# Kernel optimization log

Hardware: AMD Instinct MI355X
Metric: run time of the kernel (lower is better)

## Reference

```python
import jax, jax.numpy as jnp
import numpy as np

BETA = 0.1
GAMMA = 0.5
LABEL_SMOOTHING = 0.0
IGNORE_INDEX = -100

B, T, H, V = 8, 512, 2048, 32000  # B = 2 * num_pairs (first half chosen, second half rejected)


def setup_inputs() -> dict:
    key = jax.random.key(0)
    k1, k2, k3, k4 = jax.random.split(key, 4)
    lin_weight = jax.random.normal(k1, (V, H), dtype=jnp.float32) * 0.02
    _input = jax.random.normal(k2, (B, T, H), dtype=jnp.float32)
    target = jax.random.randint(k3, (B, T), 0, V, dtype=jnp.int64)
    # sprinkle some ignore_index positions like padded labels
    pad = jax.random.uniform(k4, (B, T)) < 0.1
    target = jnp.where(pad, IGNORE_INDEX, target)
    bias = jax.random.normal(k4, (V,), dtype=jnp.float32) * 0.02
    return {"lin_weight": lin_weight, "_input": _input, "target": target, "bias": bias}


def reference(lin_weight, _input, target, bias):
    # fused linear -> log_softmax over vocab
    logits = jnp.einsum("bth,vh->btv", _input, lin_weight) + bias  # (B, T, V)
    logps = jax.nn.log_softmax(logits.astype(jnp.float32), axis=-1)
    # gather target log-probs, masking ignore_index
    mask = (target != IGNORE_INDEX)
    tgt = jnp.where(mask, target, 0)
    per_token_logps = jnp.take_along_axis(logps, tgt[..., None], axis=-1)[..., 0]
    per_token_logps = per_token_logps * mask  # (B, T)
    # SimPO uses length-normalized (average) sequence log-prob
    avg_logps = per_token_logps.sum(-1) / jnp.maximum(mask.sum(-1), 1)  # (B,)
    n_pairs = B // 2
    chosen_logps = avg_logps[:n_pairs]
    rejected_logps = avg_logps[n_pairs:]
    d = BETA * (chosen_logps - rejected_logps) - GAMMA
    loss = (-jax.nn.log_sigmoid(d) * (1.0 - LABEL_SMOOTHING)
            - jax.nn.log_sigmoid(-d) * LABEL_SMOOTHING).sum() / n_pairs
    return loss
```

## Files before the change

### kernel.cpp

```cpp
#include <hip/hip_runtime.h>
#include <stdint.h>
#include <math.h>

constexpr int Bb = 8, Tt = 512, Hh = 2048, Vv = 32000;
constexpr int M = Bb * Tt;
constexpr int K = Hh;
constexpr int N = Vv;
constexpr int NB = N / 128;
constexpr int BK = 32;
constexpr int KITERS = K / BK;
constexpr int IGNORE = -100;

typedef __attribute__((ext_vector_type(8))) short bf16x8;
typedef __attribute__((ext_vector_type(4))) float f32x4;

__device__ inline void gld16(const void* g, const void* l) {
  __builtin_amdgcn_global_load_lds(
      (const __attribute__((address_space(1))) uint32_t*)g,
      (__attribute__((address_space(3))) uint32_t*)l, 16, 0, 0);
}

__device__ inline unsigned short f2bf(float f) {
  union { float f; unsigned u; } x; x.f = f;
  unsigned r = x.u + 0x7fffu + ((x.u >> 16) & 1u);
  return (unsigned short)(r >> 16);
}

__global__ void cast_bf16_kernel(const float* __restrict__ src,
                                 unsigned short* __restrict__ dst, int n4) {
  int i = blockIdx.x * blockDim.x + threadIdx.x;
  int stride = gridDim.x * blockDim.x;
  const float4* s4 = (const float4*)src;
  ushort4* d4 = (ushort4*)dst;
  for (; i < n4; i += stride) {
    float4 v = s4[i];
    ushort4 o;
    o.x = f2bf(v.x); o.y = f2bf(v.y); o.z = f2bf(v.z); o.w = f2bf(v.w);
    d4[i] = o;
  }
}

__global__ __launch_bounds__(256, 4)
void gemm_stats(const unsigned short* __restrict__ X,
                const unsigned short* __restrict__ W,
                const float* __restrict__ bias,
                const int* __restrict__ tgt,
                float* __restrict__ m_part,
                float* __restrict__ s_part,
                float* __restrict__ tlogit) {
  __shared__ __align__(16) unsigned short As0[128 * BK];
  __shared__ __align__(16) unsigned short As1[128 * BK];
  __shared__ __align__(16) unsigned short Bs0[128 * BK];
  __shared__ __align__(16) unsigned short Bs1[128 * BK];
  __shared__ float red_m[2][128];
  __shared__ float red_s[2][128];

  const int tid = threadIdx.x;
  const int lane = tid & 63;
  const int wid = tid >> 6;
  const int waveM = wid >> 1;
  const int waveN = wid & 1;
  const int q = lane >> 4;
  const int c = lane & 15;
  const int bm = blockIdx.x;
  const int bn = blockIdx.y;

  const int strow = tid >> 2;
  const int schunk = (lane & 3) ^ ((lane >> 2) & 3);
  const unsigned short* gA = X + (size_t)(bm * 128 + strow) * K + schunk * 8;
  const unsigned short* gB = W + (size_t)(bn * 128 + strow) * K + schunk * 8;
  const int dRow = wid * 16;

  int offA[4], offB[4];
#pragma unroll
  for (int i = 0; i < 4; ++i) {
    const int rA = waveM * 64 + i * 16 + c;
    const int rB = waveN * 64 + i * 16 + c;
    offA[i] = rA * BK + ((q ^ (rA & 3)) * 8);
    offB[i] = rB * BK + ((q ^ (rB & 3)) * 8);
  }

  f32x4 acc[4][4];
#pragma unroll
  for (int i = 0; i < 4; ++i)
#pragma unroll
    for (int j = 0; j < 4; ++j) acc[i][j] = (f32x4){0.f, 0.f, 0.f, 0.f};

  auto stage = [&](unsigned short* Ad, unsigned short* Bd, int tile) {
    const size_t k0 = (size_t)tile * BK;
#pragma unroll
    for (int j = 0; j < 2; ++j) {
      gld16(gA + (size_t)j * 64 * K + k0, Ad + (j * 64 + dRow) * BK);
      gld16(gB + (size_t)j * 64 * K + k0, Bd + (j * 64 + dRow) * BK);
    }
  };
  auto compute = [&](const unsigned short* Asb, const unsigned short* Bsb) {
    bf16x8 af[4], bfr[4];
#pragma unroll
    for (int i = 0; i < 4; ++i) {
      af[i]  = *(const bf16x8*)(Asb + offA[i]);
      bfr[i] = *(const bf16x8*)(Bsb + offB[i]);
    }
#pragma unroll
    for (int mi = 0; mi < 4; ++mi)
#pragma unroll
      for (int ni = 0; ni < 4; ++ni)
        acc[mi][ni] = __builtin_amdgcn_mfma_f32_16x16x32_bf16(
            af[mi], bfr[ni], acc[mi][ni], 0, 0, 0);
  };

  stage(As0, Bs0, 0);

  for (int i2 = 0; i2 < KITERS / 2 - 1; ++i2) {
    __syncthreads();
    stage(As1, Bs1, 2 * i2 + 1);
    compute(As0, Bs0);
    __syncthreads();
    stage(As0, Bs0, 2 * i2 + 2);
    compute(As1, Bs1);
  }
  __syncthreads();
  stage(As1, Bs1, KITERS - 1);
  compute(As0, Bs0);
  __syncthreads();
  compute(As1, Bs1);

  const int colBase = bn * 128 + waveN * 64;
  float bvals[4];
#pragma unroll
  for (int ni = 0; ni < 4; ++ni) bvals[ni] = bias[colBase + ni * 16 + c];

#pragma unroll
  for (int mi = 0; mi < 4; ++mi) {
    const int rowBase = bm * 128 + waveM * 64 + mi * 16 + q * 4;
#pragma unroll
    for (int reg = 0; reg < 4; ++reg) {
      const int grow = rowBase + reg;
      const int t = tgt[grow];
      float v[4];
      float mloc = -3.4e38f;
#pragma unroll
      for (int ni = 0; ni < 4; ++ni) {
        v[ni] = acc[mi][ni][reg] + bvals[ni];
        mloc = fmaxf(mloc, v[ni]);
        const int gn = colBase + ni * 16 + c;
        if (gn == t) tlogit[grow] = v[ni];
      }
#pragma unroll
      for (int off = 1; off < 16; off <<= 1) mloc = fmaxf(mloc, __shfl_xor(mloc, off));
      float sloc = 0.f;
#pragma unroll
      for (int ni = 0; ni < 4; ++ni) sloc += __expf(v[ni] - mloc);
#pragma unroll
      for (int off = 1; off < 16; off <<= 1) sloc += __shfl_xor(sloc, off);
      if (c == 0) {
        const int lrow = waveM * 64 + mi * 16 + q * 4 + reg;
        red_m[waveN][lrow] = mloc;
        red_s[waveN][lrow] = sloc;
      }
    }
  }
  __syncthreads();
  if (tid < 128) {
    const float m0 = red_m[0][tid], m1 = red_m[1][tid];
    const float s0 = red_s[0][tid], s1 = red_s[1][tid];
    const float mx = fmaxf(m0, m1);
    const float ss = s0 * __expf(m0 - mx) + s1 * __expf(m1 - mx);
    const int grow = bm * 128 + tid;
    m_part[(size_t)grow * NB + bn] = mx;
    s_part[(size_t)grow * NB + bn] = ss;
  }
}

__global__ __launch_bounds__(256)
void combine_rows(const float* __restrict__ m_part, const float* __restrict__ s_part,
                  const float* __restrict__ tlogit, const int* __restrict__ tgt,
                  float* __restrict__ logp) {
  const int row = blockIdx.x * 4 + (threadIdx.x >> 6);
  const int lane = threadIdx.x & 63;
  const float* mrow = m_part + (size_t)row * NB;
  const float* srow = s_part + (size_t)row * NB;
  float mv[4], sv[4];
  int cnt = 0;
  float mx = -3.4e38f;
  for (int cc = lane; cc < NB; cc += 64) {
    mv[cnt] = mrow[cc]; sv[cnt] = srow[cc];
    mx = fmaxf(mx, mv[cnt]); ++cnt;
  }
#pragma unroll
  for (int off = 32; off >= 1; off >>= 1) mx = fmaxf(mx, __shfl_xor(mx, off));
  float s = 0.f;
  for (int i = 0; i < cnt; ++i) s += sv[i] * __expf(mv[i] - mx);
#pragma unroll
  for (int off = 32; off >= 1; off >>= 1) s += __shfl_xor(s, off);
  if (lane == 0) {
    const int t = tgt[row];
    logp[row] = (t == IGNORE) ? 0.f : (tlogit[row] - mx - logf(s));
  }
}

__global__ void finalize(const float* __restrict__ logp, const int* __restrict__ tgt,
                         float* __restrict__ out) {
  __shared__ float avg[8];
  const int w = threadIdx.x >> 6;
  const int lane = threadIdx.x & 63;
  float s = 0.f, cnt = 0.f;
  for (int i = lane; i < Tt; i += 64) {
    const int idx = w * Tt + i;
    s += logp[idx];
    cnt += (tgt[idx] != IGNORE) ? 1.f : 0.f;
  }
#pragma unroll
  for (int off = 32; off >= 1; off >>= 1) {
    s += __shfl_xor(s, off);
    cnt += __shfl_xor(cnt, off);
  }
  if (lane == 0) avg[w] = s / fmaxf(cnt, 1.f);
  __syncthreads();
  if (threadIdx.x == 0) {
    float loss = 0.f;
#pragma unroll
    for (int p = 0; p < 4; ++p) {
      const float d = 0.1f * (avg[p] - avg[p + 4]) - 0.5f;
      const float nl = (d > 0.f) ? log1pf(expf(-d)) : (-d + log1pf(expf(d)));
      loss += nl;
    }
    out[0] = loss * 0.25f;
  }
}

extern "C" void kernel_launch(void* const* d_in, const int* in_sizes, int n_in,
                              void* d_out, int out_size, void* d_ws, size_t ws_size,
                              hipStream_t stream) {
  const float* Wf   = (const float*)d_in[0];
  const float* Xf   = (const float*)d_in[1];
  const int*   tgt  = (const int*)d_in[2];
  const float* bias = (const float*)d_in[3];
  float* out = (float*)d_out;

  char* ws = (char*)d_ws;
  size_t off = 0;
  auto alloc = [&](size_t bytes) {
    void* p = ws + off;
    off += (bytes + 255) & ~(size_t)255;
    return p;
  };
  unsigned short* Xbf = (unsigned short*)alloc((size_t)M * K * 2);
  unsigned short* Wbf = (unsigned short*)alloc((size_t)N * K * 2);
  float* m_part = (float*)alloc((size_t)M * NB * 4);
  float* s_part = (float*)alloc((size_t)M * NB * 4);
  float* tlog   = (float*)alloc((size_t)M * 4);
  float* logp   = (float*)alloc((size_t)M * 4);

  cast_bf16_kernel<<<2048, 256, 0, stream>>>(Xf, Xbf, M * K / 4);
  cast_bf16_kernel<<<8192, 256, 0, stream>>>(Wf, Wbf, N * K / 4);

  dim3 grid(M / 128, NB);
  gemm_stats<<<grid, 256, 0, stream>>>(Xbf, Wbf, bias, tgt, m_part, s_part, tlog);

  combine_rows<<<M / 4, 256, 0, stream>>>(m_part, s_part, tlog, tgt, logp);
  finalize<<<1, 512, 0, stream>>>(logp, tgt, out);
}
```

Measured before the change: 981.3 us.

## Enlarge GEMM tile to 256x256 with 8 waves and fine-grained phased pipeline

The GEMM moves from 128x128 tiles with 4 waves to 256x256 tiles with BK=64 and 8 waves (512 threads), using dynamic shared memory for double-buffered half-K sub-tiles. The K loop is split into phases, each interleaving one async global-to-LDS load with a block of MFMAs, with explicit vmcnt waits, raw barriers and setprio to overlap memory and compute. Blocks use a 1D grid with a swizzled mapping for better L2 locality, and combine_rows now has half as many partial columns to merge. The larger tile cuts global traffic per FLOP but raises register and LDS pressure and adds fragile hand-tuned waitcnt logic.

```diff
diff --git a/kernel.cpp b/kernel.cpp
--- a/kernel.cpp
+++ b/kernel.cpp
@@ -6,18 +6,25 @@
 constexpr int M = Bb * Tt;
 constexpr int K = Hh;
 constexpr int N = Vv;
-constexpr int NB = N / 128;
-constexpr int BK = 32;
-constexpr int KITERS = K / BK;
+constexpr int BM = 256, BN = 256, BK = 64;
+constexpr int MBLK = M / BM;
+constexpr int NBLK = N / BN;
+constexpr int KTILES = K / BK;
 constexpr int IGNORE = -100;
 
 typedef __attribute__((ext_vector_type(8))) short bf16x8;
 typedef __attribute__((ext_vector_type(4))) float f32x4;
 
-__device__ inline void gld16(const void* g, const void* l) {
+__device__ inline void gld16(const void* g, void* l) {
   __builtin_amdgcn_global_load_lds(
       (const __attribute__((address_space(1))) uint32_t*)g,
       (__attribute__((address_space(3))) uint32_t*)l, 16, 0, 0);
+}
+
+__device__ __forceinline__ void barrier_f() {
+  asm volatile("" ::: "memory");
+  __builtin_amdgcn_s_barrier();
+  asm volatile("" ::: "memory");
 }
 
 __device__ inline unsigned short f2bf(float f) {
@@ -40,7 +47,39 @@
   }
 }
 
-__global__ __launch_bounds__(256, 4)
+
+template <int BUF, int KS, int MH, int VM, class STG>
+__device__ __forceinline__ void phase(const unsigned short* __restrict__ AsB,
+                                      const unsigned short* __restrict__ BsB,
+                                      const int* offA, const int* offB,
+                                      bf16x8 (&bfrag)[4], f32x4 (&acc)[8][4],
+                                      STG&& stg) {
+  const unsigned short* Ab = AsB + (BUF * 2 + KS) * 8192;
+  if (MH == 0) {
+    const unsigned short* Bp = BsB + (BUF * 2 + KS) * 8192;
+#pragma unroll
+    for (int nf = 0; nf < 4; ++nf) bfrag[nf] = *(const bf16x8*)(Bp + offB[nf]);
+  }
+  bf16x8 af[4];
+#pragma unroll
+  for (int mi = 0; mi < 4; ++mi) af[mi] = *(const bf16x8*)(Ab + offA[MH * 4 + mi]);
+  stg();
+  if (VM == 4) asm volatile("s_waitcnt vmcnt(4)" ::: "memory");
+  if (VM == 0) asm volatile("s_waitcnt vmcnt(0)" ::: "memory");
+  barrier_f();
+  asm volatile("s_waitcnt lgkmcnt(0)" ::: "memory");
+  __builtin_amdgcn_s_setprio(1);
+#pragma unroll
+  for (int mi = 0; mi < 4; ++mi)
+#pragma unroll
+    for (int nf = 0; nf < 4; ++nf)
+      acc[MH * 4 + mi][nf] = __builtin_amdgcn_mfma_f32_16x16x32_bf16(
+          af[mi], bfrag[nf], acc[MH * 4 + mi][nf], 0, 0, 0);
+  __builtin_amdgcn_s_setprio(0);
+  barrier_f();
+}
+
+__global__ __launch_bounds__(512, 2)
 void gemm_stats(const unsigned short* __restrict__ X,
                 const unsigned short* __restrict__ W,
                 const float* __restrict__ bias,
@@ -48,91 +87,95 @@
                 float* __restrict__ m_part,
                 float* __restrict__ s_part,
                 float* __restrict__ tlogit) {
-  __shared__ __align__(16) unsigned short As0[128 * BK];
-  __shared__ __align__(16) unsigned short As1[128 * BK];
-  __shared__ __align__(16) unsigned short Bs0[128 * BK];
-  __shared__ __align__(16) unsigned short Bs1[128 * BK];
-  __shared__ float red_m[2][128];
-  __shared__ float red_s[2][128];
+  extern __shared__ unsigned short smem[];
+  unsigned short* AsB = smem;
+  unsigned short* BsB = smem + 32768;
+  float* red_m = (float*)(smem + 65536);
+  float* red_s = red_m + 1024;
 
   const int tid = threadIdx.x;
   const int lane = tid & 63;
   const int wid = tid >> 6;
-  const int waveM = wid >> 1;
-  const int waveN = wid & 1;
+  const int waveM = wid >> 2;
+  const int waveN = wid & 3;
   const int q = lane >> 4;
   const int c = lane & 15;
-  const int bm = blockIdx.x;
-  const int bn = blockIdx.y;
-
-  const int strow = tid >> 2;
-  const int schunk = (lane & 3) ^ ((lane >> 2) & 3);
-  const unsigned short* gA = X + (size_t)(bm * 128 + strow) * K + schunk * 8;
-  const unsigned short* gB = W + (size_t)(bn * 128 + strow) * K + schunk * 8;
-  const int dRow = wid * 16;
-
-  int offA[4], offB[4];
-#pragma unroll
-  for (int i = 0; i < 4; ++i) {
-    const int rA = waveM * 64 + i * 16 + c;
-    const int rB = waveN * 64 + i * 16 + c;
-    offA[i] = rA * BK + ((q ^ (rA & 3)) * 8);
-    offB[i] = rB * BK + ((q ^ (rB & 3)) * 8);
-  }
-
-  f32x4 acc[4][4];
-#pragma unroll
-  for (int i = 0; i < 4; ++i)
+
+  const int swz = (blockIdx.x & 7) * (MBLK * NBLK / 8) + (blockIdx.x >> 3);
+  const int bm = swz & (MBLK - 1);
+  const int bn = swz >> 4;
+
+  const int srow = tid >> 2;
+  const int sch = (lane & 3) ^ ((lane >> 3) & 3);
+  const unsigned short* gA = X + (size_t)(bm * BM + srow) * K + sch * 8;
+  const unsigned short* gB = W + (size_t)(bn * BN + srow) * K + sch * 8;
+  unsigned short* const dA0 = AsB + wid * 512;
+  unsigned short* const dB0 = BsB + wid * 512;
+
+  auto stA = [&](int b, int h, int t) {
+    const unsigned short* s = gA + t * BK + h * 32;
+    unsigned short* d = dA0 + (b * 2 + h) * 8192;
+    gld16(s, d);
+    gld16(s + (size_t)128 * K, d + 4096);
+  };
+  auto stB = [&](int b, int h, int t) {
+    const unsigned short* s = gB + t * BK + h * 32;
+    unsigned short* d = dB0 + (b * 2 + h) * 8192;
+    gld16(s, d);
+    gld16(s + (size_t)128 * K, d + 4096);
+  };
+
+  const int chrd = (q ^ ((c >> 1) & 3)) * 8;
+  int offA[8], offB[4];
+#pragma unroll
+  for (int mf = 0; mf < 8; ++mf) offA[mf] = (waveM * 128 + mf * 16 + c) * 32 + chrd;
+#pragma unroll
+  for (int nf = 0; nf < 4; ++nf) offB[nf] = (waveN * 64 + nf * 16 + c) * 32 + chrd;
+
+  f32x4 acc[8][4];
+#pragma unroll
+  for (int i = 0; i < 8; ++i)
 #pragma unroll
     for (int j = 0; j < 4; ++j) acc[i][j] = (f32x4){0.f, 0.f, 0.f, 0.f};
-
-  auto stage = [&](unsigned short* Ad, unsigned short* Bd, int tile) {
-    const size_t k0 = (size_t)tile * BK;
-#pragma unroll
-    for (int j = 0; j < 2; ++j) {
-      gld16(gA + (size_t)j * 64 * K + k0, Ad + (j * 64 + dRow) * BK);
-      gld16(gB + (size_t)j * 64 * K + k0, Bd + (j * 64 + dRow) * BK);
-    }
-  };
-  auto compute = [&](const unsigned short* Asb, const unsigned short* Bsb) {
-    bf16x8 af[4], bfr[4];
-#pragma unroll
-    for (int i = 0; i < 4; ++i) {
-      af[i]  = *(const bf16x8*)(Asb + offA[i]);
-      bfr[i] = *(const bf16x8*)(Bsb + offB[i]);
-    }
-#pragma unroll
-    for (int mi = 0; mi < 4; ++mi)
-#pragma unroll
-      for (int ni = 0; ni < 4; ++ni)
-        acc[mi][ni] = __builtin_amdgcn_mfma_f32_16x16x32_bf16(
-            af[mi], bfr[ni], acc[mi][ni], 0, 0, 0);
-  };
-
-  stage(As0, Bs0, 0);
-
-  for (int i2 = 0; i2 < KITERS / 2 - 1; ++i2) {
-    __syncthreads();
-    stage(As1, Bs1, 2 * i2 + 1);
-    compute(As0, Bs0);
-    __syncthreads();
-    stage(As0, Bs0, 2 * i2 + 2);
-    compute(As1, Bs1);
-  }
-  __syncthreads();
-  stage(As1, Bs1, KITERS - 1);
-  compute(As0, Bs0);
-  __syncthreads();
-  compute(As1, Bs1);
-
-  const int colBase = bn * 128 + waveN * 64;
+  bf16x8 bfrag[4];
+
+  stA(0, 0, 0); stB(0, 0, 0);
+  stA(0, 1, 0); stB(0, 1, 0);
+  stA(1, 0, 1); stB(1, 0, 1);
+  asm volatile("s_waitcnt vmcnt(4)" ::: "memory");
+  barrier_f();
+
+  for (int i = 0; i < KTILES / 2 - 1; ++i) {
+    const int t0 = 2 * i;
+    phase<0, 0, 0, -1>(AsB, BsB, offA, offB, bfrag, acc, [&] { stA(1, 1, t0 + 1); });
+    phase<0, 0, 1, -1>(AsB, BsB, offA, offB, bfrag, acc, [&] { stB(1, 1, t0 + 1); });
+    phase<0, 1, 0, -1>(AsB, BsB, offA, offB, bfrag, acc, [&] { stA(0, 0, t0 + 2); });
+    phase<0, 1, 1,  4>(AsB, BsB, offA, offB, bfrag, acc, [&] { stB(0, 0, t0 + 2); });
+    phase<1, 0, 0, -1>(AsB, BsB, offA, offB, bfrag, acc, [&] { stA(0, 1, t0 + 2); });
+    phase<1, 0, 1, -1>(AsB, BsB, offA, offB, bfrag, acc, [&] { stB(0, 1, t0 + 2); });
+    phase<1, 1, 0, -1>(AsB, BsB, offA, offB, bfrag, acc, [&] { stA(1, 0, t0 + 3); });
+    phase<1, 1, 1,  4>(AsB, BsB, offA, offB, bfrag, acc, [&] { stB(1, 0, t0 + 3); });
+  }
+  {
+    auto nop = [&] {};
+    phase<0, 0, 0, -1>(AsB, BsB, offA, offB, bfrag, acc, [&] { stA(1, 1, KTILES - 1); });
+    phase<0, 0, 1, -1>(AsB, BsB, offA, offB, bfrag, acc, [&] { stB(1, 1, KTILES - 1); });
+    phase<0, 1, 0, -1>(AsB, BsB, offA, offB, bfrag, acc, nop);
+    phase<0, 1, 1,  0>(AsB, BsB, offA, offB, bfrag, acc, nop);
+    phase<1, 0, 0, -1>(AsB, BsB, offA, offB, bfrag, acc, nop);
+    phase<1, 0, 1, -1>(AsB, BsB, offA, offB, bfrag, acc, nop);
+    phase<1, 1, 0, -1>(AsB, BsB, offA, offB, bfrag, acc, nop);
+    phase<1, 1, 1, -1>(AsB, BsB, offA, offB, bfrag, acc, nop);
+  }
+
+  const int colBase = bn * BN + waveN * 64;
   float bvals[4];
 #pragma unroll
-  for (int ni = 0; ni < 4; ++ni) bvals[ni] = bias[colBase + ni * 16 + c];
-
-#pragma unroll
-  for (int mi = 0; mi < 4; ++mi) {
-    const int rowBase = bm * 128 + waveM * 64 + mi * 16 + q * 4;
+  for (int nf = 0; nf < 4; ++nf) bvals[nf] = bias[colBase + nf * 16 + c];
+
+#pragma unroll
+  for (int mf = 0; mf < 8; ++mf) {
+    const int rowBase = bm * BM + waveM * 128 + mf * 16 + q * 4;
 #pragma unroll
     for (int reg = 0; reg < 4; ++reg) {
       const int grow = rowBase + reg;
@@ -140,35 +183,35 @@
       float v[4];
       float mloc = -3.4e38f;
 #pragma unroll
-      for (int ni = 0; ni < 4; ++ni) {
-        v[ni] = acc[mi][ni][reg] + bvals[ni];
-        mloc = fmaxf(mloc, v[ni]);
-        const int gn = colBase + ni * 16 + c;
-        if (gn == t) tlogit[grow] = v[ni];
+      for (int nf = 0; nf < 4; ++nf) {
+        v[nf] = acc[mf][nf][reg] + bvals[nf];
+        mloc = fmaxf(mloc, v[nf]);
+        if (colBase + nf * 16 + c == t) tlogit[grow] = v[nf];
       }
 #pragma unroll
       for (int off = 1; off < 16; off <<= 1) mloc = fmaxf(mloc, __shfl_xor(mloc, off));
       float sloc = 0.f;
 #pragma unroll
-      for (int ni = 0; ni < 4; ++ni) sloc += __expf(v[ni] - mloc);
+      for (int nf = 0; nf < 4; ++nf) sloc += __expf(v[nf] - mloc);
 #pragma unroll
       for (int off = 1; off < 16; off <<= 1) sloc += __shfl_xor(sloc, off);
       if (c == 0) {
-        const int lrow = waveM * 64 + mi * 16 + q * 4 + reg;
-        red_m[waveN][lrow] = mloc;
-        red_s[waveN][lrow] = sloc;
+        const int lrow = waveM * 128 + mf * 16 + q * 4 + reg;
+        red_m[waveN * 256 + lrow] = mloc;
+        red_s[waveN * 256 + lrow] = sloc;
       }
     }
   }
   __syncthreads();
-  if (tid < 128) {
-    const float m0 = red_m[0][tid], m1 = red_m[1][tid];
-    const float s0 = red_s[0][tid], s1 = red_s[1][tid];
-    const float mx = fmaxf(m0, m1);
-    const float ss = s0 * __expf(m0 - mx) + s1 * __expf(m1 - mx);
-    const int grow = bm * 128 + tid;
-    m_part[(size_t)grow * NB + bn] = mx;
-    s_part[(size_t)grow * NB + bn] = ss;
+  if (tid < 256) {
+    const float m0 = red_m[tid],       m1 = red_m[256 + tid];
+    const float m2 = red_m[512 + tid], m3 = red_m[768 + tid];
+    const float mx = fmaxf(fmaxf(m0, m1), fmaxf(m2, m3));
+    const float ss = red_s[tid] * __expf(m0 - mx) + red_s[256 + tid] * __expf(m1 - mx) +
+                     red_s[512 + tid] * __expf(m2 - mx) + red_s[768 + tid] * __expf(m3 - mx);
+    const int grow = bm * BM + tid;
+    m_part[(size_t)grow * NBLK + bn] = mx;
+    s_part[(size_t)grow * NBLK + bn] = ss;
   }
 }
 
@@ -178,19 +221,17 @@
                   float* __restrict__ logp) {
   const int row = blockIdx.x * 4 + (threadIdx.x >> 6);
   const int lane = threadIdx.x & 63;
-  const float* mrow = m_part + (size_t)row * NB;
-  const float* srow = s_part + (size_t)row * NB;
-  float mv[4], sv[4];
-  int cnt = 0;
-  float mx = -3.4e38f;
-  for (int cc = lane; cc < NB; cc += 64) {
-    mv[cnt] = mrow[cc]; sv[cnt] = srow[cc];
-    mx = fmaxf(mx, mv[cnt]); ++cnt;
-  }
+  const float* mrow = m_part + (size_t)row * NBLK;
+  const float* srow = s_part + (size_t)row * NBLK;
+  const bool v1 = (lane + 64) < NBLK;
+  const float m0 = mrow[lane];
+  const float s0 = srow[lane];
+  const float m1 = v1 ? mrow[lane + 64] : -3.4e38f;
+  const float s1 = v1 ? srow[lane + 64] : 0.f;
+  float mx = fmaxf(m0, m1);
 #pragma unroll
   for (int off = 32; off >= 1; off >>= 1) mx = fmaxf(mx, __shfl_xor(mx, off));
-  float s = 0.f;
-  for (int i = 0; i < cnt; ++i) s += sv[i] * __expf(mv[i] - mx);
+  float s = s0 * __expf(m0 - mx) + s1 * __expf(m1 - mx);
 #pragma unroll
   for (int off = 32; off >= 1; off >>= 1) s += __shfl_xor(s, off);
   if (lane == 0) {
@@ -247,16 +288,18 @@
   };
   unsigned short* Xbf = (unsigned short*)alloc((size_t)M * K * 2);
   unsigned short* Wbf = (unsigned short*)alloc((size_t)N * K * 2);
-  float* m_part = (float*)alloc((size_t)M * NB * 4);
-  float* s_part = (float*)alloc((size_t)M * NB * 4);
+  float* m_part = (float*)alloc((size_t)M * NBLK * 4);
+  float* s_part = (float*)alloc((size_t)M * NBLK * 4);
   float* tlog   = (float*)alloc((size_t)M * 4);
   float* logp   = (float*)alloc((size_t)M * 4);
 
   cast_bf16_kernel<<<2048, 256, 0, stream>>>(Xf, Xbf, M * K / 4);
   cast_bf16_kernel<<<8192, 256, 0, stream>>>(Wf, Wbf, N * K / 4);
 
-  dim3 grid(M / 128, NB);
-  gemm_stats<<<grid, 256, 0, stream>>>(Xbf, Wbf, bias, tgt, m_part, s_part, tlog);
+  constexpr size_t SMEM = 2u * 2u * 256u * 32u * 2u * 2u
+                        + 2u * 4u * 256u * 4u;
+  gemm_stats<<<dim3(MBLK * NBLK), dim3(512), SMEM, stream>>>(
+      Xbf, Wbf, bias, tgt, m_part, s_part, tlog);
 
   combine_rows<<<M / 4, 256, 0, stream>>>(m_part, s_part, tlog, tgt, logp);
   finalize<<<1, 512, 0, stream>>>(logp, tgt, out);
```

New measurement: 908.0 us. 7.5% less time.
